# Optimization experiments

Measured on AMD Instinct MI355X. Metric: run time of the kernel, lower is better.

The kernel has to match this reference:

```python
import jax, jax.numpy as jnp
import numpy as np

B, C, H, W = 16, 128, 32, 32
CHOICES, OUT_C, OH, OW = 4, 128, 32, 32
INIT_WEIGHTS = [0.25, 0.25, 0.25, 0.25]
INIT_STD = 0.01


def setup_inputs() -> dict:
    key = jax.random.key(0)
    ks = jax.random.split(key, 6)
    x = jax.random.normal(ks[0], (B, C, H, W), dtype=jnp.float32)
    # 1x1 conv1d weights == dense matrices [out, in]; xavier-normal-ish scale
    Wq = jax.random.normal(ks[1], (C, C), dtype=jnp.float32) * (1.0 / np.sqrt(C))
    Wk = jax.random.normal(ks[2], (C, C), dtype=jnp.float32) * (1.0 / np.sqrt(C))
    Wv = jax.random.normal(ks[3], (CHOICES * OUT_C, C), dtype=jnp.float32) * (1.0 / np.sqrt(C))
    gamma = jnp.ones((1,), dtype=jnp.float32)  # learnable scalar (0 at init; use 1 to exercise math)
    # mask init: per-choice mean = init_weights[i] * out_choices, std = init_std
    means = jnp.asarray([w * CHOICES for w in INIT_WEIGHTS], dtype=jnp.float32)
    mask = jax.random.normal(ks[4], (1, OUT_C, OH, OW, CHOICES), dtype=jnp.float32) * INIT_STD + means
    return {"x": x, "Wq": Wq, "Wk": Wk, "Wv": Wv, "gamma": gamma, "mask": mask}


def reference(x, Wq, Wk, Wv, gamma, mask):
    b, c, h, w = x.shape
    n = h * w
    x2 = x.reshape(b, c, n)                                   # [b, C, N]
    f = jnp.einsum('oc,bcn->bon', Wq, x2)                     # query  [b, C, N]
    g = jnp.einsum('oc,bcn->bon', Wk, x2)                     # key    [b, C, N]
    hv = jnp.einsum('oc,bcn->bon', Wv, x2)                    # value  [b, CHOICES*OUT_C, N]
    # beta = softmax(f^T g) over dim 1 (rows), per torch code
    scores = jnp.einsum('bcn,bcm->bnm', f, g)                 # [b, N, N]
    beta = jax.nn.softmax(scores, axis=1)
    out = gamma * jnp.einsum('bkn,bnm->bkm', hv, beta)        # [b, CHOICES*OUT_C, N]
    out = out.reshape(b, CHOICES, OUT_C, OH, OW)              # no resize: H==OH, W==OW
    out = jnp.transpose(out, (0, 2, 3, 4, 1))                 # [b, OUT_C, OH, OW, CHOICES]
    return out + mask
```

## Files before the change

### kernel.cpp

```cpp
#include <hip/hip_runtime.h>

#define B 16
#define C 128
#define NN 1024
#define KV 512
#define CHO 4

typedef _Float16 f16x8 __attribute__((ext_vector_type(8)));
typedef float f32x4 __attribute__((ext_vector_type(4)));

__device__ __forceinline__ unsigned short f2h(float v) {
  _Float16 h = (_Float16)v;
  return __builtin_bit_cast(unsigned short, h);
}
__device__ __forceinline__ unsigned int packh2(float a, float b) {
  return (unsigned int)f2h(a) | ((unsigned int)f2h(b) << 16);
}
__device__ __forceinline__ f16x8 ldcvt8(const float* __restrict__ p) {
  float4 a = *reinterpret_cast<const float4*>(p);
  float4 b = *reinterpret_cast<const float4*>(p + 4);
  f16x8 r;
  r[0] = (_Float16)a.x; r[1] = (_Float16)a.y; r[2] = (_Float16)a.z; r[3] = (_Float16)a.w;
  r[4] = (_Float16)b.x; r[5] = (_Float16)b.y; r[6] = (_Float16)b.z; r[7] = (_Float16)b.w;
  return r;
}

__global__ __launch_bounds__(256, 4) void proj_kernel(
    const float* __restrict__ x, const float* __restrict__ Wq,
    const float* __restrict__ Wk, const float* __restrict__ Wv,
    unsigned short* __restrict__ fT, unsigned short* __restrict__ gT,
    unsigned short* __restrict__ hv)
{
  int wg = blockIdx.x;
  wg = (wg & 7) * 384 + (wg >> 3);
  const int b   = wg / 192;
  const int rem = wg % 192;
  const int rt  = rem % 12;
  const int n0  = (rem / 12) * 64;

  __shared__ __align__(16) unsigned short XT[64][136];

  const int t = threadIdx.x;
  const int w = t >> 6, l = t & 63, lg = l >> 4, lm = l & 15;

  {
    const float* xb = x + (size_t)b * C * NN;
    #pragma unroll
    for (int i = 0; i < 8; ++i) {
      int flat = t + i * 256;
      int c  = flat >> 4;
      int ng = flat & 15;
      float4 v = *reinterpret_cast<const float4*>(xb + (size_t)c * NN + n0 + ng * 4);
      XT[ng * 4 + 0][c] = f2h(v.x);
      XT[ng * 4 + 1][c] = f2h(v.y);
      XT[ng * 4 + 2][c] = f2h(v.z);
      XT[ng * 4 + 3][c] = f2h(v.w);
    }
  }
  __syncthreads();

  if (rt < 4) {
    const float* Wsrc = (rt < 2) ? Wq : Wk;
    unsigned short* dst = (rt < 2) ? fT : gT;
    const int c0 = (rt & 1) * 64;
    const int r  = c0 + 16 * w + lm;
    f16x8 af[4];
    #pragma unroll
    for (int c4 = 0; c4 < 4; ++c4)
      af[c4] = ldcvt8(Wsrc + (size_t)r * C + c4 * 32 + lg * 8);
    #pragma unroll
    for (int nt4 = 0; nt4 < 4; ++nt4) {
      f32x4 acc = {0.f, 0.f, 0.f, 0.f};
      #pragma unroll
      for (int c4 = 0; c4 < 4; ++c4) {
        f16x8 xb = *reinterpret_cast<const f16x8*>(&XT[16 * nt4 + lm][c4 * 32 + lg * 8]);
        acc = __builtin_amdgcn_mfma_f32_16x16x32_f16(af[c4], xb, acc, 0, 0, 0);
      }
      int n = n0 + 16 * nt4 + lm;
      ushort4 o = { f2h(acc[0]), f2h(acc[1]), f2h(acc[2]), f2h(acc[3]) };
      *reinterpret_cast<ushort4*>(dst + ((size_t)(b * NN) + n) * C + c0 + 16 * w + 4 * lg) = o;
    }
  } else {
    const int kk = (rt - 4) * 64 + 16 * w + lm;
    f16x8 wb[4];
    #pragma unroll
    for (int c4 = 0; c4 < 4; ++c4)
      wb[c4] = ldcvt8(Wv + (size_t)kk * C + c4 * 32 + lg * 8);
    #pragma unroll
    for (int nt4 = 0; nt4 < 4; ++nt4) {
      f32x4 acc = {0.f, 0.f, 0.f, 0.f};
      #pragma unroll
      for (int c4 = 0; c4 < 4; ++c4) {
        f16x8 xa = *reinterpret_cast<const f16x8*>(&XT[16 * nt4 + lm][c4 * 32 + lg * 8]);
        acc = __builtin_amdgcn_mfma_f32_16x16x32_f16(xa, wb[c4], acc, 0, 0, 0);
      }
      ushort4 o = { f2h(acc[0]), f2h(acc[1]), f2h(acc[2]), f2h(acc[3]) };
      *reinterpret_cast<ushort4*>(hv + ((size_t)(b * KV) + kk) * NN + n0 + 16 * nt4 + 4 * lg) = o;
    }
  }
}

__global__ __launch_bounds__(256, 1) void attn_kernel(
    const unsigned short* __restrict__ fT, const unsigned short* __restrict__ gT,
    const unsigned short* __restrict__ hv, const float* __restrict__ gamma,
    const float* __restrict__ mask, float* __restrict__ out)
{
  int wg = blockIdx.x;
  wg = (wg & 7) * 32 + (wg >> 3);
  const int b  = wg >> 4;
  const int m0 = (wg & 15) * 64;

  const int t = threadIdx.x;
  const int w = t >> 6, l = t & 63, lg = l >> 4, lm = l & 15;

  __shared__ __align__(16) unsigned short P_lds[2][64][72];
  __shared__ float resc_s[2][64];
  __shared__ float lsum_s[64];

  f16x8 qf[4];
  {
    const unsigned short* qp = gT + ((size_t)(b * NN) + m0 + 16 * w + lm) * C + lg * 8;
    #pragma unroll
    for (int c4 = 0; c4 < 4; ++c4)
      qf[c4] = *reinterpret_cast<const f16x8*>(qp + c4 * 32);
  }

  f32x4 acc[8][4];
  #pragma unroll
  for (int kt = 0; kt < 8; ++kt)
    #pragma unroll
    for (int mt = 0; mt < 4; ++mt)
      acc[kt][mt] = (f32x4){0.f, 0.f, 0.f, 0.f};

  float M = -3.0e38f, Lpart = 0.f;

  const unsigned short* kp = fT + ((size_t)(b * NN) + lm) * C + lg * 8;
  const unsigned short* vp = hv + ((size_t)(b * KV) + 128 * w + lm) * NN + lg * 8;

  #pragma unroll 1
  for (int it = 0; it < 16; ++it) {
    const int n0  = it * 64;
    const int cur = it & 1;

    f16x8 vf[8][2];
    #pragma unroll
    for (int kt = 0; kt < 8; ++kt) {
      vf[kt][0] = *reinterpret_cast<const f16x8*>(vp + (size_t)(16 * kt) * NN + n0);
      vf[kt][1] = *reinterpret_cast<const f16x8*>(vp + (size_t)(16 * kt) * NN + n0 + 32);
    }

    f32x4 st[4];
    #pragma unroll
    for (int j = 0; j < 4; ++j) st[j] = (f32x4){0.f, 0.f, 0.f, 0.f};
    #pragma unroll
    for (int c4 = 0; c4 < 4; ++c4) {
      #pragma unroll
      for (int j = 0; j < 4; ++j) {
        f16x8 kf = *reinterpret_cast<const f16x8*>(kp + (size_t)(n0 + 16 * j) * C + c4 * 32);
        st[j] = __builtin_amdgcn_mfma_f32_16x16x32_f16(kf, qf[c4], st[j], 0, 0, 0);
      }
    }

    float cmax = -3.0e38f;
    #pragma unroll
    for (int j = 0; j < 4; ++j)
      cmax = fmaxf(cmax, fmaxf(fmaxf(st[j][0], st[j][1]), fmaxf(st[j][2], st[j][3])));
    cmax = fmaxf(cmax, __shfl_xor(cmax, 16, 64));
    cmax = fmaxf(cmax, __shfl_xor(cmax, 32, 64));
    float r = 1.0f;
    if (!__all(cmax <= M + 8.0f)) {
      float newM = fmaxf(M, cmax);
      r = __expf(M - newM);
      M = newM;
      Lpart *= r;
    }
    float p[16];
    float ls = 0.f;
    #pragma unroll
    for (int j = 0; j < 4; ++j) {
      p[4 * j + 0] = __expf(st[j][0] - M);
      p[4 * j + 1] = __expf(st[j][1] - M);
      p[4 * j + 2] = __expf(st[j][2] - M);
      p[4 * j + 3] = __expf(st[j][3] - M);
      ls += (p[4 * j] + p[4 * j + 1]) + (p[4 * j + 2] + p[4 * j + 3]);
    }
    Lpart += ls;
    if (lg == 0) resc_s[cur][16 * w + lm] = r;
    {
      unsigned short* prow = &P_lds[cur][16 * w + lm][0];
      #pragma unroll
      for (int j = 0; j < 4; ++j) {
        *(unsigned int*)(prow + 16 * j + 4 * lg)     = packh2(p[4 * j],     p[4 * j + 1]);
        *(unsigned int*)(prow + 16 * j + 4 * lg + 2) = packh2(p[4 * j + 2], p[4 * j + 3]);
      }
    }
    __syncthreads();

    float rr0 = resc_s[cur][lm],      rr1 = resc_s[cur][16 + lm],
          rr2 = resc_s[cur][32 + lm], rr3 = resc_s[cur][48 + lm];
    if (!__all((rr0 == 1.f) & (rr1 == 1.f) & (rr2 == 1.f) & (rr3 == 1.f))) {
      #pragma unroll
      for (int kt = 0; kt < 8; ++kt) {
        acc[kt][0] *= rr0; acc[kt][1] *= rr1;
        acc[kt][2] *= rr2; acc[kt][3] *= rr3;
      }
    }

    f16x8 pt[4][2];
    #pragma unroll
    for (int mt = 0; mt < 4; ++mt) {
      pt[mt][0] = *reinterpret_cast<const f16x8*>(&P_lds[cur][16 * mt + lm][8 * lg]);
      pt[mt][1] = *reinterpret_cast<const f16x8*>(&P_lds[cur][16 * mt + lm][32 + 8 * lg]);
    }

    #pragma unroll
    for (int kt = 0; kt < 8; ++kt) {
      #pragma unroll
      for (int mt = 0; mt < 4; ++mt) {
        acc[kt][mt] = __builtin_amdgcn_mfma_f32_16x16x32_f16(vf[kt][0], pt[mt][0], acc[kt][mt], 0, 0, 0);
        acc[kt][mt] = __builtin_amdgcn_mfma_f32_16x16x32_f16(vf[kt][1], pt[mt][1], acc[kt][mt], 0, 0, 0);
      }
    }
  }

  float Lp = Lpart;
  Lp += __shfl_xor(Lp, 16, 64);
  Lp += __shfl_xor(Lp, 32, 64);
  __syncthreads();
  if (lg == 0) lsum_s[16 * w + lm] = Lp;
  __syncthreads();

  const float gam = gamma[0];
  float scv[4] = { gam / lsum_s[lm],      gam / lsum_s[16 + lm],
                   gam / lsum_s[32 + lm], gam / lsum_s[48 + lm] };

  #pragma unroll
  for (int kt = 0; kt < 8; ++kt) {
    #pragma unroll
    for (int mt = 0; mt < 4; ++mt) {
      int m = m0 + 16 * mt + lm;
      #pragma unroll
      for (int reg = 0; reg < 4; ++reg) {
        int oc = 16 * kt + 4 * lg + reg;
        float v = acc[kt][mt][reg] * scv[mt] + mask[((size_t)oc * NN + m) * CHO + w];
        out[(((size_t)(b * 128 + oc)) * NN + m) * CHO + w] = v;
      }
    }
  }
}

extern "C" void kernel_launch(void* const* d_in, const int* in_sizes, int n_in,
                              void* d_out, int out_size, void* d_ws, size_t ws_size,
                              hipStream_t stream) {
  const float* x     = (const float*)d_in[0];
  const float* Wq    = (const float*)d_in[1];
  const float* Wk    = (const float*)d_in[2];
  const float* Wv    = (const float*)d_in[3];
  const float* gamma = (const float*)d_in[4];
  const float* mask  = (const float*)d_in[5];
  float* out = (float*)d_out;

  unsigned short* fT = (unsigned short*)d_ws;
  unsigned short* gT = fT + (size_t)B * NN * C;
  unsigned short* hv = gT + (size_t)B * NN * C;

  proj_kernel<<<dim3(3072), 256, 0, stream>>>(x, Wq, Wk, Wv, fT, gT, hv);
  attn_kernel<<<dim3(256), 256, 0, stream>>>(fT, gT, hv, gamma, mask, out);
}
```

Baseline: 103.5 us.

## Stage key tiles in LDS via async global_load_lds double buffering

```diff
diff --git a/kernel.cpp b/kernel.cpp
--- a/kernel.cpp
+++ b/kernel.cpp
@@ -23,6 +23,14 @@
   r[0] = (_Float16)a.x; r[1] = (_Float16)a.y; r[2] = (_Float16)a.z; r[3] = (_Float16)a.w;
   r[4] = (_Float16)b.x; r[5] = (_Float16)b.y; r[6] = (_Float16)b.z; r[7] = (_Float16)b.w;
   return r;
+}
+__device__ __forceinline__ f32x4 MFMA(f16x8 a, f16x8 b, f32x4 c) {
+  return __builtin_amdgcn_mfma_f32_16x16x32_f16(a, b, c, 0, 0, 0);
+}
+__device__ __forceinline__ void gld_lds16(const void* g, void* l) {
+  __builtin_amdgcn_global_load_lds(
+      (const __attribute__((address_space(1))) void*)g,
+      (__attribute__((address_space(3))) void*)l, 16, 0, 0);
 }
 
 __global__ __launch_bounds__(256, 4) void proj_kernel(
@@ -74,7 +82,7 @@
       #pragma unroll
       for (int c4 = 0; c4 < 4; ++c4) {
         f16x8 xb = *reinterpret_cast<const f16x8*>(&XT[16 * nt4 + lm][c4 * 32 + lg * 8]);
-        acc = __builtin_amdgcn_mfma_f32_16x16x32_f16(af[c4], xb, acc, 0, 0, 0);
+        acc = MFMA(af[c4], xb, acc);
       }
       int n = n0 + 16 * nt4 + lm;
       ushort4 o = { f2h(acc[0]), f2h(acc[1]), f2h(acc[2]), f2h(acc[3]) };
@@ -92,7 +100,7 @@
       #pragma unroll
       for (int c4 = 0; c4 < 4; ++c4) {
         f16x8 xa = *reinterpret_cast<const f16x8*>(&XT[16 * nt4 + lm][c4 * 32 + lg * 8]);
-        acc = __builtin_amdgcn_mfma_f32_16x16x32_f16(xa, wb[c4], acc, 0, 0, 0);
+        acc = MFMA(xa, wb[c4], acc);
       }
       ushort4 o = { f2h(acc[0]), f2h(acc[1]), f2h(acc[2]), f2h(acc[3]) };
       *reinterpret_cast<ushort4*>(hv + ((size_t)(b * KV) + kk) * NN + n0 + 16 * nt4 + 4 * lg) = o;
@@ -100,7 +108,7 @@
   }
 }
 
-__global__ __launch_bounds__(256, 1) void attn_kernel(
+__global__ __launch_bounds__(256, 2) void attn_kernel(
     const unsigned short* __restrict__ fT, const unsigned short* __restrict__ gT,
     const unsigned short* __restrict__ hv, const float* __restrict__ gamma,
     const float* __restrict__ mask, float* __restrict__ out)
@@ -113,6 +121,7 @@
   const int t = threadIdx.x;
   const int w = t >> 6, l = t & 63, lg = l >> 4, lm = l & 15;
 
+  __shared__ __align__(16) unsigned short Klds[2][64][128];
   __shared__ __align__(16) unsigned short P_lds[2][64][72];
   __shared__ float resc_s[2][64];
   __shared__ float lsum_s[64];
@@ -134,31 +143,55 @@
 
   float M = -3.0e38f, Lpart = 0.f;
 
-  const unsigned short* kp = fT + ((size_t)(b * NN) + lm) * C + lg * 8;
+  const char* fTb = (const char*)(fT + (size_t)(b * NN) * C);
   const unsigned short* vp = hv + ((size_t)(b * KV) + 128 * w + lm) * NN + lg * 8;
+
+  #pragma unroll
+  for (int i = 0; i < 4; ++i) {
+    int slot = 4 * i + w;
+    int row  = slot * 4 + (l >> 4);
+    int colb = (l & 15) * 16;
+    gld_lds16(fTb + (size_t)row * 256 + (colb ^ ((row & 7) << 4)),
+              (char*)&Klds[0][0][0] + slot * 1024);
+  }
+  __syncthreads();
 
   #pragma unroll 1
   for (int it = 0; it < 16; ++it) {
+    const int cur = it & 1, nxt = cur ^ 1;
     const int n0  = it * 64;
-    const int cur = it & 1;
+    const int n1  = ((it + 1) & 15) * 64;
+
+    #pragma unroll
+    for (int i = 0; i < 4; ++i) {
+      int slot = 4 * i + w;
+      int row  = slot * 4 + (l >> 4);
+      int colb = (l & 15) * 16;
+      gld_lds16(fTb + (size_t)(n1 + row) * 256 + (colb ^ ((row & 7) << 4)),
+                (char*)&Klds[nxt][0][0] + slot * 1024);
+    }
+
+    f32x4 st[4];
+    #pragma unroll
+    for (int j = 0; j < 4; ++j) st[j] = (f32x4){0.f, 0.f, 0.f, 0.f};
+    #pragma unroll
+    for (int j = 0; j < 4; ++j) {
+      const char* kbase = (const char*)&Klds[cur][0][0] + (16 * j + lm) * 256;
+      f16x8 kfr[4];
+      #pragma unroll
+      for (int c4 = 0; c4 < 4; ++c4)
+        kfr[c4] = *reinterpret_cast<const f16x8*>(
+            kbase + ((c4 * 64 + lg * 16) ^ ((lm & 7) << 4)));
+      #pragma unroll
+      for (int c4 = 0; c4 < 4; ++c4)
+        st[j] = MFMA(kfr[c4], qf[c4], st[j]);
+    }
 
     f16x8 vf[8][2];
     #pragma unroll
     for (int kt = 0; kt < 8; ++kt) {
       vf[kt][0] = *reinterpret_cast<const f16x8*>(vp + (size_t)(16 * kt) * NN + n0);
       vf[kt][1] = *reinterpret_cast<const f16x8*>(vp + (size_t)(16 * kt) * NN + n0 + 32);
-    }
-
-    f32x4 st[4];
-    #pragma unroll
-    for (int j = 0; j < 4; ++j) st[j] = (f32x4){0.f, 0.f, 0.f, 0.f};
-    #pragma unroll
-    for (int c4 = 0; c4 < 4; ++c4) {
-      #pragma unroll
-      for (int j = 0; j < 4; ++j) {
-        f16x8 kf = *reinterpret_cast<const f16x8*>(kp + (size_t)(n0 + 16 * j) * C + c4 * 32);
-        st[j] = __builtin_amdgcn_mfma_f32_16x16x32_f16(kf, qf[c4], st[j], 0, 0, 0);
-      }
     }
 
     float cmax = -3.0e38f;
@@ -174,15 +207,14 @@
       M = newM;
       Lpart *= r;
     }
-    float p[16];
     float ls = 0.f;
     #pragma unroll
     for (int j = 0; j < 4; ++j) {
-      p[4 * j + 0] = __expf(st[j][0] - M);
-      p[4 * j + 1] = __expf(st[j][1] - M);
-      p[4 * j + 2] = __expf(st[j][2] - M);
-      p[4 * j + 3] = __expf(st[j][3] - M);
-      ls += (p[4 * j] + p[4 * j + 1]) + (p[4 * j + 2] + p[4 * j + 3]);
+      st[j][0] = __expf(st[j][0] - M);
+      st[j][1] = __expf(st[j][1] - M);
+      st[j][2] = __expf(st[j][2] - M);
+      st[j][3] = __expf(st[j][3] - M);
+      ls += (st[j][0] + st[j][1]) + (st[j][2] + st[j][3]);
     }
     Lpart += ls;
     if (lg == 0) resc_s[cur][16 * w + lm] = r;
@@ -190,10 +222,11 @@
       unsigned short* prow = &P_lds[cur][16 * w + lm][0];
       #pragma unroll
       for (int j = 0; j < 4; ++j) {
-        *(unsigned int*)(prow + 16 * j + 4 * lg)     = packh2(p[4 * j],     p[4 * j + 1]);
-        *(unsigned int*)(prow + 16 * j + 4 * lg + 2) = packh2(p[4 * j + 2], p[4 * j + 3]);
-      }
-    }
+        *(unsigned int*)(prow + 16 * j + 4 * lg)     = packh2(st[j][0], st[j][1]);
+        *(unsigned int*)(prow + 16 * j + 4 * lg + 2) = packh2(st[j][2], st[j][3]);
+      }
+    }
+
     __syncthreads();
 
     float rr0 = resc_s[cur][lm],      rr1 = resc_s[cur][16 + lm],
@@ -205,28 +238,24 @@
         acc[kt][2] *= rr2; acc[kt][3] *= rr3;
       }
     }
-
     f16x8 pt[4][2];
     #pragma unroll
     for (int mt = 0; mt < 4; ++mt) {
       pt[mt][0] = *reinterpret_cast<const f16x8*>(&P_lds[cur][16 * mt + lm][8 * lg]);
       pt[mt][1] = *reinterpret_cast<const f16x8*>(&P_lds[cur][16 * mt + lm][32 + 8 * lg]);
     }
-
-    #pragma unroll
-    for (int kt = 0; kt < 8; ++kt) {
+    #pragma unroll
+    for (int kt = 0; kt < 8; ++kt)
       #pragma unroll
       for (int mt = 0; mt < 4; ++mt) {
-        acc[kt][mt] = __builtin_amdgcn_mfma_f32_16x16x32_f16(vf[kt][0], pt[mt][0], acc[kt][mt], 0, 0, 0);
-        acc[kt][mt] = __builtin_amdgcn_mfma_f32_16x16x32_f16(vf[kt][1], pt[mt][1], acc[kt][mt], 0, 0, 0);
-      }
-    }
+        acc[kt][mt] = MFMA(vf[kt][0], pt[mt][0], acc[kt][mt]);
+        acc[kt][mt] = MFMA(vf[kt][1], pt[mt][1], acc[kt][mt]);
+      }
   }
 
   float Lp = Lpart;
   Lp += __shfl_xor(Lp, 16, 64);
   Lp += __shfl_xor(Lp, 32, 64);
-  __syncthreads();
   if (lg == 0) lsum_s[16 * w + lm] = Lp;
   __syncthreads();
 
```

Measured after the change: 118.0 us. 1.14x slower.

## Split attention value channels across four workgroups per query tile

Applied to the files above, without the earlier changes.

```diff
diff --git a/kernel.cpp b/kernel.cpp
--- a/kernel.cpp
+++ b/kernel.cpp
@@ -23,6 +23,9 @@
   r[0] = (_Float16)a.x; r[1] = (_Float16)a.y; r[2] = (_Float16)a.z; r[3] = (_Float16)a.w;
   r[4] = (_Float16)b.x; r[5] = (_Float16)b.y; r[6] = (_Float16)b.z; r[7] = (_Float16)b.w;
   return r;
+}
+__device__ __forceinline__ f32x4 MFMA(f16x8 a, f16x8 b, f32x4 c) {
+  return __builtin_amdgcn_mfma_f32_16x16x32_f16(a, b, c, 0, 0, 0);
 }
 
 __global__ __launch_bounds__(256, 4) void proj_kernel(
@@ -74,7 +77,7 @@
       #pragma unroll
       for (int c4 = 0; c4 < 4; ++c4) {
         f16x8 xb = *reinterpret_cast<const f16x8*>(&XT[16 * nt4 + lm][c4 * 32 + lg * 8]);
-        acc = __builtin_amdgcn_mfma_f32_16x16x32_f16(af[c4], xb, acc, 0, 0, 0);
+        acc = MFMA(af[c4], xb, acc);
       }
       int n = n0 + 16 * nt4 + lm;
       ushort4 o = { f2h(acc[0]), f2h(acc[1]), f2h(acc[2]), f2h(acc[3]) };
@@ -92,7 +95,7 @@
       #pragma unroll
       for (int c4 = 0; c4 < 4; ++c4) {
         f16x8 xa = *reinterpret_cast<const f16x8*>(&XT[16 * nt4 + lm][c4 * 32 + lg * 8]);
-        acc = __builtin_amdgcn_mfma_f32_16x16x32_f16(xa, wb[c4], acc, 0, 0, 0);
+        acc = MFMA(xa, wb[c4], acc);
       }
       ushort4 o = { f2h(acc[0]), f2h(acc[1]), f2h(acc[2]), f2h(acc[3]) };
       *reinterpret_cast<ushort4*>(hv + ((size_t)(b * KV) + kk) * NN + n0 + 16 * nt4 + 4 * lg) = o;
@@ -100,15 +103,17 @@
   }
 }
 
-__global__ __launch_bounds__(256, 1) void attn_kernel(
+__global__ __launch_bounds__(256, 2) void attn_kernel(
     const unsigned short* __restrict__ fT, const unsigned short* __restrict__ gT,
     const unsigned short* __restrict__ hv, const float* __restrict__ gamma,
     const float* __restrict__ mask, float* __restrict__ out)
 {
   int wg = blockIdx.x;
-  wg = (wg & 7) * 32 + (wg >> 3);
-  const int b  = wg >> 4;
-  const int m0 = (wg & 15) * 64;
+  wg = (wg & 7) * 128 + (wg >> 3);
+  const int b   = wg >> 6;
+  const int rem = wg & 63;
+  const int m0  = (rem >> 2) * 64;
+  const int g   = rem & 3;
 
   const int t = threadIdx.x;
   const int w = t >> 6, l = t & 63, lg = l >> 4, lm = l & 15;
@@ -125,9 +130,9 @@
       qf[c4] = *reinterpret_cast<const f16x8*>(qp + c4 * 32);
   }
 
-  f32x4 acc[8][4];
+  f32x4 acc[2][4];
   #pragma unroll
-  for (int kt = 0; kt < 8; ++kt)
+  for (int kt = 0; kt < 2; ++kt)
     #pragma unroll
     for (int mt = 0; mt < 4; ++mt)
       acc[kt][mt] = (f32x4){0.f, 0.f, 0.f, 0.f};
@@ -135,16 +140,16 @@
   float M = -3.0e38f, Lpart = 0.f;
 
   const unsigned short* kp = fT + ((size_t)(b * NN) + lm) * C + lg * 8;
-  const unsigned short* vp = hv + ((size_t)(b * KV) + 128 * w + lm) * NN + lg * 8;
+  const unsigned short* vp = hv + ((size_t)(b * KV) + 128 * g + 32 * w + lm) * NN + lg * 8;
 
   #pragma unroll 1
   for (int it = 0; it < 16; ++it) {
     const int n0  = it * 64;
     const int cur = it & 1;
 
-    f16x8 vf[8][2];
-    #pragma unroll
-    for (int kt = 0; kt < 8; ++kt) {
+    f16x8 vf[2][2];
+    #pragma unroll
+    for (int kt = 0; kt < 2; ++kt) {
       vf[kt][0] = *reinterpret_cast<const f16x8*>(vp + (size_t)(16 * kt) * NN + n0);
       vf[kt][1] = *reinterpret_cast<const f16x8*>(vp + (size_t)(16 * kt) * NN + n0 + 32);
     }
@@ -157,7 +162,7 @@
       #pragma unroll
       for (int j = 0; j < 4; ++j) {
         f16x8 kf = *reinterpret_cast<const f16x8*>(kp + (size_t)(n0 + 16 * j) * C + c4 * 32);
-        st[j] = __builtin_amdgcn_mfma_f32_16x16x32_f16(kf, qf[c4], st[j], 0, 0, 0);
+        st[j] = MFMA(kf, qf[c4], st[j]);
       }
     }
 
@@ -174,15 +179,14 @@
       M = newM;
       Lpart *= r;
     }
-    float p[16];
     float ls = 0.f;
     #pragma unroll
     for (int j = 0; j < 4; ++j) {
-      p[4 * j + 0] = __expf(st[j][0] - M);
-      p[4 * j + 1] = __expf(st[j][1] - M);
-      p[4 * j + 2] = __expf(st[j][2] - M);
-      p[4 * j + 3] = __expf(st[j][3] - M);
-      ls += (p[4 * j] + p[4 * j + 1]) + (p[4 * j + 2] + p[4 * j + 3]);
+      st[j][0] = __expf(st[j][0] - M);
+      st[j][1] = __expf(st[j][1] - M);
+      st[j][2] = __expf(st[j][2] - M);
+      st[j][3] = __expf(st[j][3] - M);
+      ls += (st[j][0] + st[j][1]) + (st[j][2] + st[j][3]);
     }
     Lpart += ls;
     if (lg == 0) resc_s[cur][16 * w + lm] = r;
@@ -190,8 +194,8 @@
       unsigned short* prow = &P_lds[cur][16 * w + lm][0];
       #pragma unroll
       for (int j = 0; j < 4; ++j) {
-        *(unsigned int*)(prow + 16 * j + 4 * lg)     = packh2(p[4 * j],     p[4 * j + 1]);
-        *(unsigned int*)(prow + 16 * j + 4 * lg + 2) = packh2(p[4 * j + 2], p[4 * j + 3]);
+        *(unsigned int*)(prow + 16 * j + 4 * lg)     = packh2(st[j][0], st[j][1]);
+        *(unsigned int*)(prow + 16 * j + 4 * lg + 2) = packh2(st[j][2], st[j][3]);
       }
     }
     __syncthreads();
@@ -200,7 +204,7 @@
           rr2 = resc_s[cur][32 + lm], rr3 = resc_s[cur][48 + lm];
     if (!__all((rr0 == 1.f) & (rr1 == 1.f) & (rr2 == 1.f) & (rr3 == 1.f))) {
       #pragma unroll
-      for (int kt = 0; kt < 8; ++kt) {
+      for (int kt = 0; kt < 2; ++kt) {
         acc[kt][0] *= rr0; acc[kt][1] *= rr1;
         acc[kt][2] *= rr2; acc[kt][3] *= rr3;
       }
@@ -214,13 +218,12 @@
     }
 
     #pragma unroll
-    for (int kt = 0; kt < 8; ++kt) {
+    for (int kt = 0; kt < 2; ++kt)
       #pragma unroll
       for (int mt = 0; mt < 4; ++mt) {
-        acc[kt][mt] = __builtin_amdgcn_mfma_f32_16x16x32_f16(vf[kt][0], pt[mt][0], acc[kt][mt], 0, 0, 0);
-        acc[kt][mt] = __builtin_amdgcn_mfma_f32_16x16x32_f16(vf[kt][1], pt[mt][1], acc[kt][mt], 0, 0, 0);
-      }
-    }
+        acc[kt][mt] = MFMA(vf[kt][0], pt[mt][0], acc[kt][mt]);
+        acc[kt][mt] = MFMA(vf[kt][1], pt[mt][1], acc[kt][mt]);
+      }
   }
 
   float Lp = Lpart;
@@ -235,15 +238,15 @@
                    gam / lsum_s[32 + lm], gam / lsum_s[48 + lm] };
 
   #pragma unroll
-  for (int kt = 0; kt < 8; ++kt) {
+  for (int kt = 0; kt < 2; ++kt) {
     #pragma unroll
     for (int mt = 0; mt < 4; ++mt) {
       int m = m0 + 16 * mt + lm;
       #pragma unroll
       for (int reg = 0; reg < 4; ++reg) {
-        int oc = 16 * kt + 4 * lg + reg;
-        float v = acc[kt][mt][reg] * scv[mt] + mask[((size_t)oc * NN + m) * CHO + w];
-        out[(((size_t)(b * 128 + oc)) * NN + m) * CHO + w] = v;
+        int oc = 32 * w + 16 * kt + 4 * lg + reg;
+        float v = acc[kt][mt][reg] * scv[mt] + mask[((size_t)oc * NN + m) * CHO + g];
+        out[(((size_t)(b * 128 + oc)) * NN + m) * CHO + g] = v;
       }
     }
   }
@@ -265,5 +268,5 @@
   unsigned short* hv = gT + (size_t)B * NN * C;
 
   proj_kernel<<<dim3(3072), 256, 0, stream>>>(x, Wq, Wk, Wv, fT, gT, hv);
-  attn_kernel<<<dim3(256), 256, 0, stream>>>(fT, gT, hv, gamma, mask, out);
-}
+  attn_kernel<<<dim3(1024), 256, 0, stream>>>(fT, gT, hv, gamma, mask, out);
+}
```

After: 184.2 us. 1.78x slower.
